# Kernel optimization log

Hardware: AMD Instinct MI355X
Metric: run time of the kernel (lower is better)

## Reference

```python
import jax, jax.numpy as jnp
import numpy as np

B, T, C = 4, 2048, 1024
H, D = 16, 64  # num_heads, head_size; H*D == C


def setup_inputs() -> dict:
    key = jax.random.key(0)
    kx, kq, kk, kv = jax.random.split(key, 4)
    x = jax.random.normal(kx, (B, T, C), dtype=jnp.float32)
    # Per-head bias-free Q/K/V projection weights, stacked over heads.
    # Scale like torch Linear default init (~1/sqrt(fan_in)).
    s = 1.0 / np.sqrt(C)
    Wq = jax.random.normal(kq, (H, C, D), dtype=jnp.float32) * s
    Wk = jax.random.normal(kk, (H, C, D), dtype=jnp.float32) * s
    Wv = jax.random.normal(kv, (H, C, D), dtype=jnp.float32) * s
    return {"x": x, "Wq": Wq, "Wk": Wk, "Wv": Wv}


def reference(x, Wq, Wk, Wv):
    # Batched equivalent of the per-head Python loop:
    # each head: q = x @ Wq[h]; k = x @ Wk[h]; v = x @ Wv[h]
    q = jnp.einsum("btc,hcd->bhtd", x, Wq)
    k = jnp.einsum("bsc,hcd->bhsd", x, Wk)
    v = jnp.einsum("bsc,hcd->bhsd", x, Wv)
    scale = 1.0 / jnp.sqrt(jnp.asarray(D, dtype=x.dtype))
    scores = jnp.einsum("bhtd,bhsd->bhts", q, k) * scale  # [B,H,T,T]
    causal = jnp.tril(jnp.ones((T, T), dtype=bool))
    scores = jnp.where(causal[None, None], scores, jnp.asarray(-jnp.inf, scores.dtype))
    attn = jax.nn.softmax(scores, axis=-1)  # dropout=0 (inference)
    out = jnp.einsum("bhts,bhsd->bhtd", attn, v)
    # Concatenate heads on the last dim (head 0 first), matching torch.cat.
    return out.transpose(0, 2, 1, 3).reshape(B, T, H * D)
```

## Files before the change

### kernel.cpp

```cpp
#include <hip/hip_runtime.h>
#include <hip/hip_bf16.h>


typedef __attribute__((ext_vector_type(8))) short short8;
typedef __attribute__((ext_vector_type(4))) float f32x4;
typedef __attribute__((ext_vector_type(16))) float f32x16;

#define XB_OFF  64
#define WT_OFF  (64 + 8388608)
#define QKV_OFF (64 + 8388608 + 3145728)

__device__ __forceinline__ short f2bf(float f) {
    union { float f; unsigned u; } un; un.f = f;
    unsigned r = un.u + 0x7fffu + ((un.u >> 16) & 1u);
    return (short)(r >> 16);
}
__device__ __forceinline__ float bf2f(short v) {
    union { unsigned u; float f; } un; un.u = ((unsigned)(unsigned short)v) << 16;
    return un.f;
}
__device__ __forceinline__ unsigned cvtpk_bf16(float lo, float hi) {
    unsigned r;
    asm("v_cvt_pk_bf16_f32 %0, %1, %2" : "=v"(r) : "v"(lo), "v"(hi));
    return r;
}
__device__ __forceinline__ float fast_exp2(float x) {
    return __builtin_amdgcn_exp2f(x);
}

__device__ __forceinline__ int swz(int row, int colByte) {
    return row * 144 + (colByte ^ ((row & 56) << 1));
}

#define GLOAD16(gsrc, ldst)                                                       \
    __builtin_amdgcn_global_load_lds(                                             \
        (const __attribute__((address_space(1))) void*)(gsrc),                    \
        (__attribute__((address_space(3))) void*)(ldst), 16, 0, 0)

__global__ __launch_bounds__(256) void detect_dtype(const unsigned short* __restrict__ xs,
                                                    int* __restrict__ flag) {
    __shared__ int red[256];
    int t = threadIdx.x, cnt = 0;
    for (int i = t; i < 8192; i += 256) {
        unsigned e = (xs[i] >> 7) & 0xFFu;
        if (e >= 0xC0u) cnt++;
    }
    red[t] = cnt;
    __syncthreads();
    for (int s = 128; s > 0; s >>= 1) { if (t < s) red[t] += red[t + s]; __syncthreads(); }
    if (t == 0) flag[0] = (red[0] > 16) ? 1 : 0;
}

__global__ __launch_bounds__(256) void convert_x(const void* __restrict__ xin,
                                                 const int* __restrict__ flag,
                                                 short* __restrict__ xb) {
    const bool isf = (flag[0] != 0);
    const int n8 = 8388608 / 8;
    int i = blockIdx.x * 256 + threadIdx.x;
    const int stride = gridDim.x * 256;
    for (; i < n8; i += stride) {
        short8 v;
        if (isf) {
            const f32x4* xf = (const f32x4*)xin + i * 2;
            f32x4 a = xf[0], b = xf[1];
#pragma unroll
            for (int j = 0; j < 4; ++j) { v[j] = f2bf(a[j]); v[4 + j] = f2bf(b[j]); }
        } else {
            v = ((const short8*)xin)[i];
        }
        ((short8*)xb)[i] = v;
    }
}

__global__ __launch_bounds__(256) void transpose_w(const void* __restrict__ W0,
                                                   const void* __restrict__ W1,
                                                   const void* __restrict__ W2,
                                                   const int* __restrict__ flag,
                                                   short* __restrict__ Wt) {
    __shared__ short tile[64][72];
    const bool isf = (flag[0] != 0);
    const int s  = blockIdx.z;
    const void* W = (s == 0) ? W0 : (s == 1) ? W1 : W2;
    const int h  = blockIdx.y;
    const int c0 = blockIdx.x * 64;
    const int t  = threadIdx.x;
#pragma unroll
    for (int p = 0; p < 2; ++p) {
        int f8 = t + p * 256;
        int r  = f8 >> 3;
        int c8 = (f8 & 7) * 8;
        size_t base = (size_t)(h * 1024 + c0 + r) * 64 + c8;
        short8 v;
        if (isf) {
            const float* wf = (const float*)W + base;
#pragma unroll
            for (int j = 0; j < 8; ++j) v[j] = f2bf(wf[j]);
        } else {
            v = *(const short8*)((const short*)W + base);
        }
        *(short8*)&tile[r][c8] = v;
    }
    __syncthreads();
#pragma unroll
    for (int p = 0; p < 2; ++p) {
        int f8 = t + p * 256;
        int d  = f8 >> 3;
        int c8 = (f8 & 7) * 8;
        short8 v;
#pragma unroll
        for (int j = 0; j < 8; ++j) v[j] = tile[c8 + j][d];
        *(short8*)(Wt + (size_t)((s * 16 + h) * 64 + d) * 1024 + c0 + c8) = v;
    }
}

__global__ __launch_bounds__(256) void qkv_gemm(const short* __restrict__ xb,
                                                const short* __restrict__ Wt,
                                                short* __restrict__ qkv) {
    __shared__ short As[128 * 32];
    __shared__ short Bs[128 * 32];
    const int m0 = blockIdx.x * 128;
    const int n0 = blockIdx.y * 128;
    const int tid = threadIdx.x;
    const int wv = tid >> 6, ln = tid & 63;
    const int lr = ln & 15, lg = ln >> 4;
    const int wr = wv >> 1, wc = wv & 1;
    const int s = n0 >> 10;
    const int b = m0 >> 11;
    const float qs = (s == 0) ? 0.18033688f : 1.0f;

    const int srow = ln >> 2;
    const int sgrp = ((ln & 3) ^ ((ln >> 3) & 3)) * 8;
    const int roff = (lg ^ ((lr >> 1) & 3)) * 8;

    f32x4 acc[4][4] = {};
    const short* Abase = xb + (size_t)m0 * 1024;
    const short* Bbase = Wt + (size_t)n0 * 1024;

    for (int k0 = 0; k0 < 1024; k0 += 32) {
        const int r0 = wv * 16, r1 = 64 + wv * 16;
        GLOAD16(Abase + (size_t)(r0 + srow) * 1024 + k0 + sgrp, As + r0 * 32);
        GLOAD16(Abase + (size_t)(r1 + srow) * 1024 + k0 + sgrp, As + r1 * 32);
        GLOAD16(Bbase + (size_t)(r0 + srow) * 1024 + k0 + sgrp, Bs + r0 * 32);
        GLOAD16(Bbase + (size_t)(r1 + srow) * 1024 + k0 + sgrp, Bs + r1 * 32);
        __syncthreads();
        short8 af[4], bfr[4];
#pragma unroll
        for (int i = 0; i < 4; ++i)
            af[i] = *(const short8*)&As[(wr * 64 + i * 16 + lr) * 32 + roff];
#pragma unroll
        for (int i = 0; i < 4; ++i)
            bfr[i] = *(const short8*)&Bs[(wc * 64 + i * 16 + lr) * 32 + roff];
#pragma unroll
        for (int mi = 0; mi < 4; ++mi)
#pragma unroll
            for (int ni = 0; ni < 4; ++ni)
                acc[mi][ni] = __builtin_amdgcn_mfma_f32_16x16x32_bf16(af[mi], bfr[ni], acc[mi][ni], 0, 0, 0);
        __syncthreads();
    }

#pragma unroll
    for (int ni = 0; ni < 4; ++ni) {
        const int colbase = n0 + wc * 64 + ni * 16;
        const int h  = (colbase >> 6) & 15;
        const int d0 = colbase & 63;
        short* orow = qkv + (size_t)((s * 4 + b) * 16 + h) * 2048 * 64 + d0 + lr;
#pragma unroll
        for (int mi = 0; mi < 4; ++mi)
#pragma unroll
            for (int r = 0; r < 4; ++r) {
                int t = (m0 & 2047) + wr * 64 + mi * 16 + lg * 4 + r;
                orow[(size_t)t * 64] = f2bf(acc[mi][ni][r] * qs);
            }
    }
}

#define BUILD_PW(s, stx, base) {                                             \
    unsigned P01 = cvtpk_bf16(stx[base + 0], stx[base + 1]);                 \
    unsigned P23 = cvtpk_bf16(stx[base + 2], stx[base + 3]);                 \
    unsigned P45 = cvtpk_bf16(stx[base + 4], stx[base + 5]);                 \
    unsigned P67 = cvtpk_bf16(stx[base + 6], stx[base + 7]);                 \
    asm volatile("v_permlane32_swap_b32 %0, %1" : "+v"(P01), "+v"(P45));     \
    asm volatile("v_permlane32_swap_b32 %0, %1" : "+v"(P23), "+v"(P67));     \
    pw[s][0] = P01; pw[s][1] = P23; pw[s][2] = P45; pw[s][3] = P67;          \
}

__device__ __forceinline__ void process_tile(const char* KsB, const char* VtB,
                                             short8 a0, short8 a1, short8 a2, short8 a3,
                                             float& ls,
                                             f32x16& o0, f32x16& o1,
                                             int qg, int kv0, bool diag,
                                             int q_, int hl) {
    short8 aq[4] = {a0, a1, a2, a3};
    f32x16 st0, st1;
#pragma unroll
    for (int r = 0; r < 16; ++r) { st0[r] = -14.0f; st1[r] = -14.0f; }
    __builtin_amdgcn_s_setprio(1);
#pragma unroll
    for (int s = 0; s < 4; ++s) {
        short8 kf0 = *(const short8*)(KsB + swz(q_,      s * 32 + hl * 16));
        short8 kf1 = *(const short8*)(KsB + swz(32 + q_, s * 32 + hl * 16));
        st0 = __builtin_amdgcn_mfma_f32_32x32x16_bf16(kf0, aq[s], st0, 0, 0, 0);
        st1 = __builtin_amdgcn_mfma_f32_32x32x16_bf16(kf1, aq[s], st1, 0, 0, 0);
    }
    __builtin_amdgcn_s_setprio(0);
    if (diag) {
#pragma unroll
        for (int r = 0; r < 16; ++r) {
            int key = kv0 + (r & 3) + 8 * (r >> 2) + 4 * hl;
            st0[r] = (key      <= qg) ? st0[r] : -1.0e30f;
            st1[r] = (key + 32 <= qg) ? st1[r] : -1.0e30f;
        }
    }
#pragma unroll
    for (int r = 0; r < 16; ++r) {
        st0[r] = fast_exp2(st0[r]);
        st1[r] = fast_exp2(st1[r]);
    }
    float tsum[8];
#pragma unroll
    for (int i = 0; i < 8; ++i)
        tsum[i] = (st0[i] + st0[i + 8]) + (st1[i] + st1[i + 8]);
    ls += ((tsum[0] + tsum[1]) + (tsum[2] + tsum[3]))
        + ((tsum[4] + tsum[5]) + (tsum[6] + tsum[7]));

    unsigned pw[4][4];
    BUILD_PW(0, st0, 0)
    BUILD_PW(1, st0, 8)
    BUILD_PW(2, st1, 0)
    BUILD_PW(3, st1, 8)
    __builtin_amdgcn_s_setprio(1);
#pragma unroll
    for (int s = 0; s < 4; ++s) {
        union { unsigned u[4]; short8 s8; } pb;
        pb.u[0] = pw[s][0]; pb.u[1] = pw[s][1]; pb.u[2] = pw[s][2]; pb.u[3] = pw[s][3];
        short8 v0 = *(const short8*)(VtB + swz(q_,      s * 32 + hl * 16));
        short8 v1 = *(const short8*)(VtB + swz(32 + q_, s * 32 + hl * 16));
        o0 = __builtin_amdgcn_mfma_f32_32x32x16_bf16(v0, pb.s8, o0, 0, 0, 0);
        o1 = __builtin_amdgcn_mfma_f32_32x32x16_bf16(v1, pb.s8, o1, 0, 0, 0);
    }
    __builtin_amdgcn_s_setprio(0);
}

#define EPILOGUE(oA, oB, lsv, q0base) {                                           \
    __syncthreads();                                                              \
    float inv = 1.0f / (lsv);                                                     \
    const int qlocal = w * 32 + q_;                                               \
    _Pragma("unroll")                                                             \
    for (int r = 0; r < 16; r += 2) {                                             \
        int d0 = (r & 3) + 8 * (r >> 2) + 4 * hl;                                 \
        *(unsigned*)(OtB + swz(qlocal, 2 * d0)) =                                 \
            cvtpk_bf16(oA[r] * inv, oA[r + 1] * inv);                             \
        *(unsigned*)(OtB + swz(qlocal, 2 * (32 + d0))) =                          \
            cvtpk_bf16(oB[r] * inv, oB[r + 1] * inv);                             \
    }                                                                             \
    __syncthreads();                                                              \
    _Pragma("unroll")                                                             \
    for (int i2 = 0; i2 < 4; ++i2) {                                              \
        int idx = i2 * 256 + tid;                                                 \
        int row = idx >> 3, cc8 = (idx & 7) * 8;                                  \
        short8 vch = *(const short8*)(OtB + swz(row, cc8 * 2));                   \
        size_t obase = (size_t)(b * 2048 + (q0base) + row) * 1024 + h * 64 + cc8; \
        if (isf) {                                                                \
            f32x4 lo2, hi2;                                                       \
            _Pragma("unroll")                                                     \
            for (int j = 0; j < 4; ++j) { lo2[j] = bf2f(vch[j]); hi2[j] = bf2f(vch[4 + j]); } \
            *(f32x4*)((float*)outp + obase)     = lo2;                            \
            *(f32x4*)((float*)outp + obase + 4) = hi2;                            \
        } else {                                                                  \
            *(short8*)((short*)outp + obase) = vch;                               \
        }                                                                         \
    }                                                                             \
}

__global__ __launch_bounds__(256, 2) void attn(const short* __restrict__ qkv,
                                               const int* __restrict__ flag,
                                               void* __restrict__ outp) {
    __shared__ short lds_all[2 * 9216];
    const bool isf = (flag[0] != 0);
    const int L    = (int)blockIdx.x;
    const int xcd  = L & 7;
    const int s_   = L >> 3;
    const int qbl  = s_ & 7;
    const int hb   = xcd * 8 + (s_ >> 3);
    const int b    = hb >> 4;
    const int h    = hb & 15;
    const int tid = threadIdx.x;
    const int w  = tid >> 6, l = tid & 63;
    const int q_ = l & 31;
    const int hl = l >> 5;
    const size_t BHTD = (size_t)4 * 16 * 2048 * 64;
    const short* Qb = qkv + (size_t)(b * 16 + h) * 2048 * 64;
    const short* Kb = Qb + BHTD;
    const short* Vb = Qb + 2 * BHTD;

    const int qbs0 = qbl, qbs1 = 15 - qbl;
    const int nt0 = 2 * qbs0 + 2, nt1 = 2 * qbs1 + 2;
    const int qg0 = qbs0 * 128 + w * 32 + q_;
    const int qg1 = qbs1 * 128 + w * 32 + q_;

    short8 aq0[4], aq1[4];
#pragma unroll
    for (int s = 0; s < 4; ++s) {
        aq0[s] = *(const short8*)(Qb + (size_t)qg0 * 64 + s * 16 + hl * 8);
        aq1[s] = *(const short8*)(Qb + (size_t)qg1 * 64 + s * 16 + hl * 8);
    }

    float ls0 = 0.f, ls1 = 0.f;
    f32x16 o00 = {}, o01 = {}, o10 = {}, o11 = {};

    const int kr = (tid >> 3) * 2;
    const int c8 = (tid & 7) * 8;
    short8 kreg[2], vreg[2];

    {
        kreg[0] = *(const short8*)(Kb + (size_t)kr * 64 + c8);
        kreg[1] = *(const short8*)(Kb + (size_t)(kr + 1) * 64 + c8);
        vreg[0] = *(const short8*)(Vb + (size_t)kr * 64 + c8);
        vreg[1] = *(const short8*)(Vb + (size_t)(kr + 1) * 64 + c8);
        char* KsN = (char*)lds_all;
        char* VtN = KsN + 9216;
        *(short8*)(KsN + swz(kr,     c8 * 2)) = kreg[0];
        *(short8*)(KsN + swz(kr + 1, c8 * 2)) = kreg[1];
#pragma unroll
        for (int j = 0; j < 8; ++j) {
            unsigned pv = (unsigned)(unsigned short)vreg[0][j]
                        | ((unsigned)(unsigned short)vreg[1][j] << 16);
            *(unsigned*)(VtN + swz(c8 + j, kr * 2)) = pv;
        }
    }

    for (int kt = 0; kt < nt1; ++kt) {
        const char* KsB = (const char*)lds_all + (kt & 1) * 18432;
        const char* VtB = KsB + 9216;
        __syncthreads();
        if (kt + 1 < nt1) {
            const short* Kn = Kb + (size_t)(kt + 1) * 4096;
            const short* Vn = Vb + (size_t)(kt + 1) * 4096;
            kreg[0] = *(const short8*)(Kn + (size_t)kr * 64 + c8);
            kreg[1] = *(const short8*)(Kn + (size_t)(kr + 1) * 64 + c8);
            vreg[0] = *(const short8*)(Vn + (size_t)kr * 64 + c8);
            vreg[1] = *(const short8*)(Vn + (size_t)(kr + 1) * 64 + c8);
        }
        const int kv0 = kt * 64;
        process_tile(KsB, VtB, aq1[0], aq1[1], aq1[2], aq1[3], ls1,
                     o10, o11, qg1, kv0, kt >= 2 * qbs1, q_, hl);
        if (kt < nt0)
            process_tile(KsB, VtB, aq0[0], aq0[1], aq0[2], aq0[3], ls0,
                         o00, o01, qg0, kv0, kt >= 2 * qbs0, q_, hl);
        if (kt + 1 < nt1) {
            char* KsN = (char*)lds_all + ((kt + 1) & 1) * 18432;
            char* VtN = KsN + 9216;
            *(short8*)(KsN + swz(kr,     c8 * 2)) = kreg[0];
            *(short8*)(KsN + swz(kr + 1, c8 * 2)) = kreg[1];
#pragma unroll
            for (int j = 0; j < 8; ++j) {
                unsigned pv = (unsigned)(unsigned short)vreg[0][j]
                            | ((unsigned)(unsigned short)vreg[1][j] << 16);
                *(unsigned*)(VtN + swz(c8 + j, kr * 2)) = pv;
            }
        }
    }

    ls0 += __shfl_xor(ls0, 32);
    ls1 += __shfl_xor(ls1, 32);
    char* const OtB = (char*)lds_all;
    EPILOGUE(o00, o01, ls0, qbs0 * 128)
    EPILOGUE(o10, o11, ls1, qbs1 * 128)
}

extern "C" void kernel_launch(void* const* d_in, const int* in_sizes, int n_in,
                              void* d_out, int out_size, void* d_ws, size_t ws_size,
                              hipStream_t stream) {
    short* ws   = (short*)d_ws;
    int*  flag  = (int*)d_ws;
    short* xb   = ws + XB_OFF;
    short* Wt   = ws + WT_OFF;
    short* qkvb = ws + QKV_OFF;

    dim3 blk(256);
    detect_dtype<<<1, blk, 0, stream>>>((const unsigned short*)d_in[0], flag);
    convert_x<<<dim3(1024), blk, 0, stream>>>(d_in[0], flag, xb);
    transpose_w<<<dim3(16, 16, 3), blk, 0, stream>>>(d_in[1], d_in[2], d_in[3], flag, Wt);
    qkv_gemm<<<dim3(64, 24), blk, 0, stream>>>(xb, Wt, qkvb);
    attn<<<dim3(512), blk, 0, stream>>>(qkvb, flag, d_out);
}
```

Before: 133.2 us.

## Double GEMM K-tile to 64 with new LDS swizzle and XCD-aware block mapping

The QKV projection GEMM now stages 64-wide K slices in LDS instead of 32, halving the number of barrier pairs per output tile. Each slice is consumed as two MFMA substeps, and the LDS swizzle is rewritten for 128-byte rows. The grid is flattened to 1D and remapped so blocks on the same XCD share the same N-column group, which should improve L2 reuse of weight tiles. LDS per block doubles, which may reduce occupancy.

```diff
diff --git a/kernel.cpp b/kernel.cpp
--- a/kernel.cpp
+++ b/kernel.cpp
@@ -116,10 +116,16 @@
 __global__ __launch_bounds__(256) void qkv_gemm(const short* __restrict__ xb,
                                                 const short* __restrict__ Wt,
                                                 short* __restrict__ qkv) {
-    __shared__ short As[128 * 32];
-    __shared__ short Bs[128 * 32];
-    const int m0 = blockIdx.x * 128;
-    const int n0 = blockIdx.y * 128;
+    __shared__ short As[128 * 64];
+    __shared__ short Bs[128 * 64];
+    const int L   = (int)blockIdx.x;
+    const int xcd = L & 7;
+    const int t_  = L >> 3;
+    const int x   = t_ / 3;
+    const int yg  = t_ % 3;
+    const int y   = xcd * 3 + yg;
+    const int m0 = x * 128;
+    const int n0 = y * 128;
     const int tid = threadIdx.x;
     const int wv = tid >> 6, ln = tid & 63;
     const int lr = ln & 15, lg = ln >> 4;
@@ -128,33 +134,42 @@
     const int b = m0 >> 11;
     const float qs = (s == 0) ? 0.18033688f : 1.0f;
 
-    const int srow = ln >> 2;
-    const int sgrp = ((ln & 3) ^ ((ln >> 3) & 3)) * 8;
-    const int roff = (lg ^ ((lr >> 1) & 3)) * 8;
+    const int srow8 = ln >> 3;
+    const int sgrp  = ((ln & 7) ^ srow8) * 8;
+    const int rsw   = (lr & 7);
 
     f32x4 acc[4][4] = {};
     const short* Abase = xb + (size_t)m0 * 1024;
     const short* Bbase = Wt + (size_t)n0 * 1024;
 
-    for (int k0 = 0; k0 < 1024; k0 += 32) {
-        const int r0 = wv * 16, r1 = 64 + wv * 16;
-        GLOAD16(Abase + (size_t)(r0 + srow) * 1024 + k0 + sgrp, As + r0 * 32);
-        GLOAD16(Abase + (size_t)(r1 + srow) * 1024 + k0 + sgrp, As + r1 * 32);
-        GLOAD16(Bbase + (size_t)(r0 + srow) * 1024 + k0 + sgrp, Bs + r0 * 32);
-        GLOAD16(Bbase + (size_t)(r1 + srow) * 1024 + k0 + sgrp, Bs + r1 * 32);
+    for (int k0 = 0; k0 < 1024; k0 += 64) {
+#pragma unroll
+        for (int j = 0; j < 4; ++j) {
+            const int r0 = j * 32 + wv * 8;
+            GLOAD16(Abase + (size_t)(r0 + srow8) * 1024 + k0 + sgrp, As + r0 * 64);
+            GLOAD16(Bbase + (size_t)(r0 + srow8) * 1024 + k0 + sgrp, Bs + r0 * 64);
+        }
         __syncthreads();
-        short8 af[4], bfr[4];
-#pragma unroll
-        for (int i = 0; i < 4; ++i)
-            af[i] = *(const short8*)&As[(wr * 64 + i * 16 + lr) * 32 + roff];
-#pragma unroll
-        for (int i = 0; i < 4; ++i)
-            bfr[i] = *(const short8*)&Bs[(wc * 64 + i * 16 + lr) * 32 + roff];
-#pragma unroll
-        for (int mi = 0; mi < 4; ++mi)
-#pragma unroll
-            for (int ni = 0; ni < 4; ++ni)
-                acc[mi][ni] = __builtin_amdgcn_mfma_f32_16x16x32_bf16(af[mi], bfr[ni], acc[mi][ni], 0, 0, 0);
+#pragma unroll
+        for (int ks = 0; ks < 2; ++ks) {
+            short8 af[4], bfr[4];
+            const int slot = (ks * 4 + lg);
+#pragma unroll
+            for (int i = 0; i < 4; ++i) {
+                int arow = wr * 64 + i * 16 + lr;
+                af[i] = *(const short8*)((const char*)As + arow * 128 + ((slot ^ rsw) * 16));
+            }
+#pragma unroll
+            for (int i = 0; i < 4; ++i) {
+                int brow = wc * 64 + i * 16 + lr;
+                bfr[i] = *(const short8*)((const char*)Bs + brow * 128 + ((slot ^ rsw) * 16));
+            }
+#pragma unroll
+            for (int mi = 0; mi < 4; ++mi)
+#pragma unroll
+                for (int ni = 0; ni < 4; ++ni)
+                    acc[mi][ni] = __builtin_amdgcn_mfma_f32_16x16x32_bf16(af[mi], bfr[ni], acc[mi][ni], 0, 0, 0);
+        }
         __syncthreads();
     }
 
@@ -381,6 +396,6 @@
     detect_dtype<<<1, blk, 0, stream>>>((const unsigned short*)d_in[0], flag);
     convert_x<<<dim3(1024), blk, 0, stream>>>(d_in[0], flag, xb);
     transpose_w<<<dim3(16, 16, 3), blk, 0, stream>>>(d_in[1], d_in[2], d_in[3], flag, Wt);
-    qkv_gemm<<<dim3(64, 24), blk, 0, stream>>>(xb, Wt, qkvb);
+    qkv_gemm<<<dim3(1536), blk, 0, stream>>>(xb, Wt, qkvb);
     attn<<<dim3(512), blk, 0, stream>>>(qkvb, flag, d_out);
 }
```

Measured after the change: 138.5 us. 3.9% more time.
